# Performance work log

Hardware: AMD Instinct MI355X
Metric: run time of the kernel (lower is better)

The kernel has to match this reference:

```python
import jax, jax.numpy as jnp
import numpy as np

COMMITMENT_COST = 0.25


def setup_inputs() -> dict:
    key = jax.random.key(0)
    kx, ke = jax.random.split(key)
    x = jax.random.normal(kx, (16, 2048, 256), dtype=jnp.float32)
    embedding = jax.random.normal(ke, (4096, 256), dtype=jnp.float32)
    return {"x": x, "embedding": embedding}


def reference(x, embedding):
    # x: [B, T, D], embedding: [M, D]. Eval-mode VQ-EMA forward (no buffer updates).
    B, T, D = x.shape
    M = embedding.shape[0]
    x_flat = x.reshape(-1, D)  # [N, D], N = B*T

    distances = (
        jnp.sum(embedding * embedding, axis=1)[None, :]
        + jnp.sum(x_flat * x_flat, axis=1, keepdims=True)
        - 2.0 * (x_flat @ embedding.T)
    )
    indices = jnp.argmin(distances.astype(jnp.float32), axis=-1)  # [N]
    quantized = embedding[indices].reshape(x.shape)  # gather lookup, [B, T, D]

    # commitment loss, masked by nonpadding frames
    e_latent = (x - jax.lax.stop_gradient(quantized)) ** 2  # mse, reduction='none'
    nonpadding = (jnp.abs(x).sum(-1) > 0).astype(x.dtype)  # [B, T]
    e_latent_loss = (e_latent.mean(-1) * nonpadding).sum() / nonpadding.sum()
    loss = COMMITMENT_COST * e_latent_loss

    # straight-through estimator
    quantized_st = x + jax.lax.stop_gradient(quantized - x)

    # perplexity from code usage histogram (avoid materializing [N, M] one-hot)
    counts = jnp.zeros((M,), jnp.float32).at[indices].add(1.0)
    avg_probs = counts / indices.shape[0]
    perplexity = jnp.exp(-jnp.sum(avg_probs * jnp.log(avg_probs + 1e-10)))

    return quantized_st, loss, indices.reshape(B, T), perplexity
```

## Files before the change

### kernel.cpp

```cpp
#include <hip/hip_runtime.h>
#include <math.h>
#include <stdint.h>

#define D 256
#define N 32768
#define M 4096

#define LOSS_OFF 8388608
#define IDX_OFF  8388609
#define PERP_OFF 8421377

typedef _Float16 f16;
typedef _Float16 f16x8 __attribute__((ext_vector_type(8)));
typedef _Float16 f16x4 __attribute__((ext_vector_type(4)));
typedef float f32x4 __attribute__((ext_vector_type(4)));

#define WS_XH     0u
#define WS_XL     16777216u
#define WS_EH     33554432u
#define WS_EL     35651584u
#define WS_ENORM  37748736u
#define WS_COUNTS 37765120u
#define WS_IDX    37781504u
#define WS_CAND   37912576u
#define WS_LPART  38961152u
#define WS_NPART  38969344u
#define WS_NEEDED 38977536u
#define C_BLOCKS  2048

__device__ __forceinline__ void gload16(const void* g, void* l) {
    __builtin_amdgcn_global_load_lds(
        (const __attribute__((address_space(1))) uint32_t*)g,
        (__attribute__((address_space(3))) uint32_t*)l, 16, 0, 0);
}

#define MFMA16(a, b, c) __builtin_amdgcn_mfma_f32_16x16x32_f16((a), (b), (c), 0, 0, 0)

__global__ __launch_bounds__(256) void init_kernel(const float* __restrict__ emb,
                                                   float* __restrict__ enorm,
                                                   unsigned* __restrict__ counts) {
    int tid = threadIdx.x;
    int lane = tid & 63;
    int wid = tid >> 6;
    int m = blockIdx.x * 4 + wid;
    const float4* e4 = (const float4*)(emb + (size_t)m * D);
    float4 v = e4[lane];
    float s = v.x * v.x + v.y * v.y + v.z * v.z + v.w * v.w;
    #pragma unroll
    for (int off = 32; off; off >>= 1) s += __shfl_xor(s, off);
    if (lane == 0) enorm[m] = s;
    int gid = blockIdx.x * 256 + tid;
    if (gid < M) counts[gid] = 0u;
}

__global__ __launch_bounds__(256) void convert_kernel(const float* __restrict__ s,
                                                      f16* __restrict__ dh,
                                                      f16* __restrict__ dl, int n4) {
    int i = blockIdx.x * 256 + threadIdx.x;
    if (i >= n4) return;
    float4 v = ((const float4*)s)[i];
    f16 h0 = (f16)v.x, h1 = (f16)v.y, h2 = (f16)v.z, h3 = (f16)v.w;
    f16 l0 = (f16)(v.x - (float)h0), l1 = (f16)(v.y - (float)h1);
    f16 l2 = (f16)(v.z - (float)h2), l3 = (f16)(v.w - (float)h3);
    f16x4 hv; hv[0] = h0; hv[1] = h1; hv[2] = h2; hv[3] = h3;
    f16x4 lv; lv[0] = l0; lv[1] = l1; lv[2] = l2; lv[3] = l3;
    *(f16x4*)(dh + (size_t)i * 4) = hv;
    *(f16x4*)(dl + (size_t)i * 4) = lv;
}

__global__ __launch_bounds__(512) void argmin_xp(
    const f16* __restrict__ xh, const f16* __restrict__ xl,
    const f16* __restrict__ eh, const f16* __restrict__ el,
    const float* __restrict__ enorm, float2* __restrict__ cand)
{
    extern __shared__ char smem[];
    f16* Xh = (f16*)smem;
    f16* EBa = (f16*)(smem + 65536);
    float2 (*msm)[32] = (float2(*)[32])(smem + 65536);

    int tid = threadIdx.x;
    int lane = tid & 63;
    int wid = tid >> 6;
    int wr = wid >> 1;
    int wc = wid & 1;
    int b = blockIdx.x;
    int rb = (b & 7) * 32 + (b >> 5);
    int cs = (b >> 3) & 3;
    int row0 = rb * 128;
    int rxor = lane & 7;

    {
        int srow = lane >> 5, lslot = lane & 31;
        #pragma unroll
        for (int q = 0; q < 8; ++q) {
            int ch = wid * 8 + q;
            int row = ch * 2 + srow;
            int ss = lslot ^ (row & 7);
            gload16(xh + (size_t)(row0 + row) * D + ss * 8, smem + ch * 1024);
        }
    }
    {
        int srow = lane >> 3, lslot = lane & 7;
        int c0 = cs * 1024;
        #pragma unroll
        for (int q = 0; q < 2; ++q) {
            int ch = wid * 2 + q;
            int row = ch * 8 + srow;
            int ss = lslot ^ (row & 7);
            const f16* src = (ss < 4) ? eh : el;
            gload16(src + (size_t)(c0 + row) * D + (ss & 3) * 8,
                    smem + 65536 + ch * 1024);
        }
    }
    f16x8 xlr[2][8];
    #pragma unroll
    for (int i = 0; i < 2; ++i) {
        int row = row0 + wr * 32 + i * 16 + (lane & 15);
        #pragma unroll
        for (int kc = 0; kc < 8; ++kc)
            xlr[i][kc] = *(const f16x8*)(xl + (size_t)row * D + kc * 32 + (lane >> 4) * 8);
    }
    __syncthreads();

    float bestv[2][4];
    int bestc[2][4];
    #pragma unroll
    for (int i = 0; i < 2; ++i)
        #pragma unroll
        for (int r = 0; r < 4; ++r) { bestv[i][r] = 3.4e38f; bestc[i][r] = 0; }

    for (int ct = 0; ct < 8; ++ct) {
        int c0 = (cs * 8 + ct) * 128;
        f32x4 acc[2][4];
        #pragma unroll
        for (int i = 0; i < 2; ++i)
            #pragma unroll
            for (int j = 0; j < 4; ++j) acc[i][j] = (f32x4)0.0f;

        #pragma unroll
        for (int kc = 0; kc < 8; ++kc) {
            if (ct * 8 + kc < 63) {
                int t1 = ct * 8 + kc + 1;
                int ct1 = t1 >> 3, kc1 = t1 & 7, d1 = t1 & 1;
                int c01 = (cs * 8 + ct1) * 128;
                int srow = lane >> 3, lslot = lane & 7;
                #pragma unroll
                for (int q = 0; q < 2; ++q) {
                    int ch = wid * 2 + q;
                    int row = ch * 8 + srow;
                    int ss = lslot ^ (row & 7);
                    const f16* src = (ss < 4) ? eh : el;
                    gload16(src + (size_t)(c01 + row) * D + kc1 * 32 + (ss & 3) * 8,
                            smem + 65536 + d1 * 16384 + ch * 1024);
                }
            }
            {
                const f16* EB = EBa + (kc & 1) * 8192;
                f16x8 ah[2], bh[4], bl[4];
                #pragma unroll
                for (int i = 0; i < 2; ++i) {
                    int row = wr * 32 + i * 16 + (lane & 15);
                    int sl = (kc * 4 + (lane >> 4)) ^ rxor;
                    ah[i] = *(const f16x8*)(Xh + row * 256 + sl * 8);
                }
                #pragma unroll
                for (int j = 0; j < 4; ++j) {
                    int row = wc * 64 + j * 16 + (lane & 15);
                    const f16* ebr = EB + row * 64;
                    bh[j] = *(const f16x8*)(ebr + (((lane >> 4)) ^ rxor) * 8);
                    bl[j] = *(const f16x8*)(ebr + ((4 + (lane >> 4)) ^ rxor) * 8);
                }
                #pragma unroll
                for (int i = 0; i < 2; ++i)
                    #pragma unroll
                    for (int j = 0; j < 4; ++j)
                        acc[i][j] = MFMA16(ah[i], bh[j], acc[i][j]);
                #pragma unroll
                for (int i = 0; i < 2; ++i)
                    #pragma unroll
                    for (int j = 0; j < 4; ++j)
                        acc[i][j] = MFMA16(ah[i], bl[j], acc[i][j]);
                #pragma unroll
                for (int i = 0; i < 2; ++i)
                    #pragma unroll
                    for (int j = 0; j < 4; ++j)
                        acc[i][j] = MFMA16(xlr[i][kc], bh[j], acc[i][j]);
            }
            __syncthreads();
        }
        float enj[4];
        #pragma unroll
        for (int j = 0; j < 4; ++j) enj[j] = enorm[c0 + wc * 64 + j * 16 + (lane & 15)];
        #pragma unroll
        for (int i = 0; i < 2; ++i)
            #pragma unroll
            for (int j = 0; j < 4; ++j) {
                int c = c0 + wc * 64 + j * 16 + (lane & 15);
                #pragma unroll
                for (int r = 0; r < 4; ++r) {
                    float s = enj[j] - 2.0f * acc[i][j][r];
                    if (s < bestv[i][r]) { bestv[i][r] = s; bestc[i][r] = c; }
                }
            }
    }

    float rv[2][4]; int rc[2][4];
    #pragma unroll
    for (int i = 0; i < 2; ++i)
        #pragma unroll
        for (int r = 0; r < 4; ++r) {
            float v = bestv[i][r]; int c = bestc[i][r];
            #pragma unroll
            for (int off = 8; off; off >>= 1) {
                float ov = __shfl_xor(v, off);
                int oc = __shfl_xor(c, off);
                if (ov < v || (ov == v && oc < c)) { v = ov; c = oc; }
            }
            rv[i][r] = v; rc[i][r] = c;
            if ((lane & 15) == 0 && wc == 1) {
                int rloc = i * 16 + (lane >> 4) * 4 + r;
                float2 p; p.x = v; p.y = __int_as_float(c);
                msm[wr][rloc] = p;
            }
        }
    __syncthreads();
    if (wc == 0 && (lane & 15) == 0) {
        #pragma unroll
        for (int i = 0; i < 2; ++i)
            #pragma unroll
            for (int r = 0; r < 4; ++r) {
                int rloc = i * 16 + (lane >> 4) * 4 + r;
                float v = rv[i][r]; int c = rc[i][r];
                float2 o = msm[wr][rloc];
                float ov = o.x; int oc = __float_as_int(o.y);
                if (ov < v || (ov == v && oc < c)) { v = ov; c = oc; }
                float2 p; p.x = v; p.y = __int_as_float(c);
                cand[(size_t)cs * N + row0 + wr * 32 + rloc] = p;
            }
    }
}

__global__ __launch_bounds__(256) void merge_kernel(const float2* __restrict__ cand,
                                                    unsigned* __restrict__ counts,
                                                    int* __restrict__ idx_out,
                                                    float* __restrict__ idx_f) {
    int row = blockIdx.x * 256 + threadIdx.x;
    float bv = 3.4e38f; int bc = 0;
    #pragma unroll
    for (int cs = 0; cs < 4; ++cs) {
        float2 p = cand[(size_t)cs * N + row];
        int c = __float_as_int(p.y);
        if (p.x < bv || (p.x == bv && c < bc)) { bv = p.x; bc = c; }
    }
    idx_out[row] = bc;
    idx_f[row] = (float)bc;
    atomicAdd(&counts[bc], 1u);
}

#define BR 64
#define BC 128
#define BK 64
__global__ __launch_bounds__(256) void argmin_fp32(
    const float* __restrict__ x, const float* __restrict__ emb,
    const float* __restrict__ enorm, unsigned* __restrict__ counts,
    int* __restrict__ idx_out, float* __restrict__ idx_f)
{
    __shared__ float xs[BR][65];
    __shared__ float es[BC][65];
    __shared__ float en_s[BC];
    int tid = threadIdx.x;
    int ty = tid >> 4, tx = tid & 15;
    int r0 = blockIdx.x * BR;
    float bestv[4]; int bestc[4];
    #pragma unroll
    for (int i = 0; i < 4; ++i) { bestv[i] = 3.4e38f; bestc[i] = 0; }
    for (int ct = 0; ct < M / BC; ++ct) {
        int c0 = ct * BC;
        float acc[4][8];
        #pragma unroll
        for (int i = 0; i < 4; ++i)
            #pragma unroll
            for (int j = 0; j < 8; ++j) acc[i][j] = 0.0f;
        for (int kt = 0; kt < D / BK; ++kt) {
            __syncthreads();
            #pragma unroll
            for (int p = 0; p < 4; ++p) {
                int l = p * 256 + tid, r = l >> 4, k4 = l & 15;
                float4 v = *(const float4*)(x + (size_t)(r0 + r) * D + kt * BK + k4 * 4);
                xs[r][k4 * 4] = v.x; xs[r][k4 * 4 + 1] = v.y;
                xs[r][k4 * 4 + 2] = v.z; xs[r][k4 * 4 + 3] = v.w;
            }
            #pragma unroll
            for (int p = 0; p < 8; ++p) {
                int l = p * 256 + tid, r = l >> 4, k4 = l & 15;
                float4 v = *(const float4*)(emb + (size_t)(c0 + r) * D + kt * BK + k4 * 4);
                es[r][k4 * 4] = v.x; es[r][k4 * 4 + 1] = v.y;
                es[r][k4 * 4 + 2] = v.z; es[r][k4 * 4 + 3] = v.w;
            }
            if (kt == 0 && tid < BC) en_s[tid] = enorm[c0 + tid];
            __syncthreads();
            #pragma unroll 8
            for (int k = 0; k < BK; ++k) {
                float xv[4], ev[8];
                #pragma unroll
                for (int i = 0; i < 4; ++i) xv[i] = xs[ty + 16 * i][k];
                #pragma unroll
                for (int j = 0; j < 8; ++j) ev[j] = es[tx + 16 * j][k];
                #pragma unroll
                for (int i = 0; i < 4; ++i)
                    #pragma unroll
                    for (int j = 0; j < 8; ++j)
                        acc[i][j] = fmaf(xv[i], ev[j], acc[i][j]);
            }
        }
        #pragma unroll
        for (int i = 0; i < 4; ++i)
            #pragma unroll
            for (int j = 0; j < 8; ++j) {
                int c = c0 + tx + 16 * j;
                float s = en_s[tx + 16 * j] - 2.0f * acc[i][j];
                if (s < bestv[i]) { bestv[i] = s; bestc[i] = c; }
            }
    }
    #pragma unroll
    for (int i = 0; i < 4; ++i) {
        float v = bestv[i]; int c = bestc[i];
        #pragma unroll
        for (int off = 8; off; off >>= 1) {
            float ov = __shfl_xor(v, off, 16);
            int oc = __shfl_xor(c, off, 16);
            if (ov < v || (ov == v && oc < c)) { v = ov; c = oc; }
        }
        if (tx == 0) {
            int row = r0 + ty + 16 * i;
            idx_out[row] = c; idx_f[row] = (float)c;
            atomicAdd(&counts[c], 1u);
        }
    }
}

__global__ __launch_bounds__(256) void gather_kernel(
    const float* __restrict__ x, const float* __restrict__ emb,
    const int* __restrict__ idx, float* __restrict__ out,
    float* __restrict__ lpart, float* __restrict__ npart)
{
    int tid = threadIdx.x, lane = tid & 63, wid = tid >> 6;
    __shared__ float ls[4], ns[4];
    double lacc = 0.0, nacc = 0.0;
    for (int it = 0; it < 4; ++it) {
        int row = (blockIdx.x * 4 + wid) + it * (C_BLOCKS * 4);
        int c = idx[row];
        float4 xv = *(const float4*)(x + (size_t)row * D + lane * 4);
        float4 qv = *(const float4*)(emb + (size_t)c * D + lane * 4);
        float4 o;
        o.x = xv.x + (qv.x - xv.x); o.y = xv.y + (qv.y - xv.y);
        o.z = xv.z + (qv.z - xv.z); o.w = xv.w + (qv.w - xv.w);
        *(float4*)(out + (size_t)row * D + lane * 4) = o;
        float dx = xv.x - qv.x, dy = xv.y - qv.y, dz = xv.z - qv.z, dw = xv.w - qv.w;
        float ss = dx * dx + dy * dy + dz * dz + dw * dw;
        float sa = fabsf(xv.x) + fabsf(xv.y) + fabsf(xv.z) + fabsf(xv.w);
        #pragma unroll
        for (int off = 32; off; off >>= 1) {
            ss += __shfl_xor(ss, off);
            sa += __shfl_xor(sa, off);
        }
        if (sa > 0.0f) { lacc += (double)ss * (1.0 / 256.0); nacc += 1.0; }
    }
    if (lane == 0) { ls[wid] = (float)lacc; ns[wid] = (float)nacc; }
    __syncthreads();
    if (tid == 0) {
        lpart[blockIdx.x] = ls[0] + ls[1] + ls[2] + ls[3];
        npart[blockIdx.x] = ns[0] + ns[1] + ns[2] + ns[3];
    }
}

__global__ __launch_bounds__(256) void finalize_kernel(
    const unsigned* __restrict__ counts, const float* __restrict__ lpart,
    const float* __restrict__ npart, float* __restrict__ out)
{
    __shared__ double sd[256];
    __shared__ double sl[256];
    __shared__ double sn[256];
    int tid = threadIdx.x;
    double t = 0.0;
    for (int i = tid; i < M; i += 256) {
        double p = (double)counts[i] * (1.0 / 32768.0);
        t += p * log(p + 1e-10);
    }
    sd[tid] = t;
    double ln = 0.0, nn = 0.0;
    for (int i = tid; i < C_BLOCKS; i += 256) { ln += lpart[i]; nn += npart[i]; }
    sl[tid] = ln; sn[tid] = nn;
    __syncthreads();
    for (int s = 128; s; s >>= 1) {
        if (tid < s) { sd[tid] += sd[tid + s]; sl[tid] += sl[tid + s]; sn[tid] += sn[tid + s]; }
        __syncthreads();
    }
    if (tid == 0) {
        out[PERP_OFF] = (float)exp(-sd[0]);
        out[LOSS_OFF] = (float)(0.25 * sl[0] / sn[0]);
    }
}

extern "C" void kernel_launch(void* const* d_in, const int* in_sizes, int n_in,
                              void* d_out, int out_size, void* d_ws, size_t ws_size,
                              hipStream_t stream) {
    const float* x = (const float*)d_in[0];
    const float* emb = (const float*)d_in[1];
    float* out = (float*)d_out;
    char* ws = (char*)d_ws;

    float* enorm = (float*)(ws + WS_ENORM);
    unsigned* counts = (unsigned*)(ws + WS_COUNTS);
    int* idx = (int*)(ws + WS_IDX);
    float* lpart = (float*)(ws + WS_LPART);
    float* npart = (float*)(ws + WS_NPART);

    if (ws_size >= (size_t)WS_NEEDED) {
        f16* xh = (f16*)(ws + WS_XH);
        f16* xl = (f16*)(ws + WS_XL);
        f16* eh = (f16*)(ws + WS_EH);
        f16* el = (f16*)(ws + WS_EL);
        float2* cand = (float2*)(ws + WS_CAND);

        init_kernel<<<M / 4, 256, 0, stream>>>(emb, enorm, counts);
        convert_kernel<<<(N * D / 4) / 256, 256, 0, stream>>>(x, xh, xl, N * D / 4);
        convert_kernel<<<(M * D / 4) / 256, 256, 0, stream>>>(emb, eh, el, M * D / 4);
        argmin_xp<<<1024, 512, 98304, stream>>>(xh, xl, eh, el, enorm, cand);
        merge_kernel<<<N / 256, 256, 0, stream>>>(cand, counts, idx, out + IDX_OFF);
    } else {
        enorm = (float*)(ws + 0);
        counts = (unsigned*)(ws + 16384);
        idx = (int*)(ws + 32768);
        lpart = (float*)(ws + 163840);
        npart = (float*)(ws + 172032);
        init_kernel<<<M / 4, 256, 0, stream>>>(emb, enorm, counts);
        argmin_fp32<<<N / BR, 256, 0, stream>>>(x, emb, enorm, counts, idx, out + IDX_OFF);
    }
    gather_kernel<<<C_BLOCKS, 256, 0, stream>>>(x, emb, idx, out, lpart, npart);
    finalize_kernel<<<1, 256, 0, stream>>>(counts, lpart, npart, out);
}
```

Before: 322.6 us.

## Convert x to hi/lo fp16 in registers and fuse merge into gather

The argmin kernel now reads fp32 x directly and splits it into fp16 hi/lo register fragments, which removes the separate x conversion pass and its workspace traffic. The codebook tiles are staged in 128-wide K halves with double buffering across a 128KB LDS allocation, cutting the number of barriers per column tile from eight to two. The candidate merge is folded into the gather/loss kernel, which drops one launch and the intermediate index buffer. In exchange the larger LDS footprint and the extra x registers may limit occupancy despite the launch bound of 2.

```diff
diff --git a/kernel.cpp b/kernel.cpp
--- a/kernel.cpp
+++ b/kernel.cpp
@@ -68,15 +68,13 @@
     *(f16x4*)(dl + (size_t)i * 4) = lv;
 }
 
-__global__ __launch_bounds__(512) void argmin_xp(
-    const f16* __restrict__ xh, const f16* __restrict__ xl,
-    const f16* __restrict__ eh, const f16* __restrict__ el,
-    const float* __restrict__ enorm, float2* __restrict__ cand)
+__global__ __launch_bounds__(512, 2) void argmin_xr(
+    const float* __restrict__ x, const f16* __restrict__ eh,
+    const f16* __restrict__ el, const float* __restrict__ enorm,
+    float2* __restrict__ cand)
 {
     extern __shared__ char smem[];
-    f16* Xh = (f16*)smem;
-    f16* EBa = (f16*)(smem + 65536);
-    float2 (*msm)[32] = (float2(*)[32])(smem + 65536);
+    float2 (*msm)[32] = (float2(*)[32])smem;
 
     int tid = threadIdx.x;
     int lane = tid & 63;
@@ -90,35 +88,34 @@
     int rxor = lane & 7;
 
     {
-        int srow = lane >> 5, lslot = lane & 31;
         #pragma unroll
         for (int q = 0; q < 8; ++q) {
-            int ch = wid * 8 + q;
-            int row = ch * 2 + srow;
-            int ss = lslot ^ (row & 7);
-            gload16(xh + (size_t)(row0 + row) * D + ss * 8, smem + ch * 1024);
-        }
-    }
-    {
-        int srow = lane >> 3, lslot = lane & 7;
-        int c0 = cs * 1024;
-        #pragma unroll
-        for (int q = 0; q < 2; ++q) {
-            int ch = wid * 2 + q;
-            int row = ch * 8 + srow;
-            int ss = lslot ^ (row & 7);
-            const f16* src = (ss < 4) ? eh : el;
-            gload16(src + (size_t)(c0 + row) * D + (ss & 3) * 8,
-                    smem + 65536 + ch * 1024);
-        }
-    }
-    f16x8 xlr[2][8];
+            int cb = q * 8 + wid;
+            int row = (cb * 4 + (lane >> 4)) & 127;
+            int ks = ((lane & 15) ^ (row & 7)) * 8;
+            const f16* src = (cb >> 5) ? el : eh;
+            gload16(src + (size_t)(cs * 1024 + row) * D + ks, smem + cb * 1024);
+        }
+    }
+    f16x8 xhr[2][8], xlr[2][8];
     #pragma unroll
     for (int i = 0; i < 2; ++i) {
-        int row = row0 + wr * 32 + i * 16 + (lane & 15);
-        #pragma unroll
-        for (int kc = 0; kc < 8; ++kc)
-            xlr[i][kc] = *(const f16x8*)(xl + (size_t)row * D + kc * 32 + (lane >> 4) * 8);
+        const float* xr = x + (size_t)(row0 + wr * 32 + i * 16 + (lane & 15)) * D;
+        #pragma unroll
+        for (int kc = 0; kc < 8; ++kc) {
+            float4 v0 = *(const float4*)(xr + kc * 32 + (lane >> 4) * 8);
+            float4 v1 = *(const float4*)(xr + kc * 32 + (lane >> 4) * 8 + 4);
+            f16x8 h, l;
+            h[0] = (f16)v0.x; l[0] = (f16)(v0.x - (float)h[0]);
+            h[1] = (f16)v0.y; l[1] = (f16)(v0.y - (float)h[1]);
+            h[2] = (f16)v0.z; l[2] = (f16)(v0.z - (float)h[2]);
+            h[3] = (f16)v0.w; l[3] = (f16)(v0.w - (float)h[3]);
+            h[4] = (f16)v1.x; l[4] = (f16)(v1.x - (float)h[4]);
+            h[5] = (f16)v1.y; l[5] = (f16)(v1.y - (float)h[5]);
+            h[6] = (f16)v1.z; l[6] = (f16)(v1.z - (float)h[6]);
+            h[7] = (f16)v1.w; l[7] = (f16)(v1.w - (float)h[7]);
+            xhr[i][kc] = h; xlr[i][kc] = l;
+        }
     }
     __syncthreads();
 
@@ -138,53 +135,47 @@
             for (int j = 0; j < 4; ++j) acc[i][j] = (f32x4)0.0f;
 
         #pragma unroll
-        for (int kc = 0; kc < 8; ++kc) {
-            if (ct * 8 + kc < 63) {
-                int t1 = ct * 8 + kc + 1;
-                int ct1 = t1 >> 3, kc1 = t1 & 7, d1 = t1 & 1;
+        for (int kh = 0; kh < 2; ++kh) {
+            if (kh == 0 || ct < 7) {
+                int ct1 = (kh == 0) ? ct : ct + 1;
+                int kh1 = kh ^ 1;
                 int c01 = (cs * 8 + ct1) * 128;
-                int srow = lane >> 3, lslot = lane & 7;
-                #pragma unroll
-                for (int q = 0; q < 2; ++q) {
-                    int ch = wid * 2 + q;
-                    int row = ch * 8 + srow;
-                    int ss = lslot ^ (row & 7);
-                    const f16* src = (ss < 4) ? eh : el;
-                    gload16(src + (size_t)(c01 + row) * D + kc1 * 32 + (ss & 3) * 8,
-                            smem + 65536 + d1 * 16384 + ch * 1024);
+                char* dst = smem + (kh ^ 1) * 65536;
+                #pragma unroll
+                for (int q = 0; q < 8; ++q) {
+                    int cb = q * 8 + wid;
+                    int row = (cb * 4 + (lane >> 4)) & 127;
+                    int ks = (((lane & 15) ^ (row & 7)) * 8) + kh1 * 128;
+                    const f16* src = (cb >> 5) ? el : eh;
+                    gload16(src + (size_t)(c01 + row) * D + ks, dst + cb * 1024);
                 }
             }
-            {
-                const f16* EB = EBa + (kc & 1) * 8192;
-                f16x8 ah[2], bh[4], bl[4];
-                #pragma unroll
-                for (int i = 0; i < 2; ++i) {
-                    int row = wr * 32 + i * 16 + (lane & 15);
-                    int sl = (kc * 4 + (lane >> 4)) ^ rxor;
-                    ah[i] = *(const f16x8*)(Xh + row * 256 + sl * 8);
-                }
+            const f16* EB = (const f16*)(smem + kh * 65536);
+            #pragma unroll
+            for (int kq = 0; kq < 4; ++kq) {
+                f16x8 bh[4], bl[4];
                 #pragma unroll
                 for (int j = 0; j < 4; ++j) {
-                    int row = wc * 64 + j * 16 + (lane & 15);
-                    const f16* ebr = EB + row * 64;
-                    bh[j] = *(const f16x8*)(ebr + (((lane >> 4)) ^ rxor) * 8);
-                    bl[j] = *(const f16x8*)(ebr + ((4 + (lane >> 4)) ^ rxor) * 8);
+                    int brow = wc * 64 + j * 16 + (lane & 15);
+                    int sw = (kq * 4 + (lane >> 4)) ^ rxor;
+                    bh[j] = *(const f16x8*)(EB + brow * 128 + sw * 8);
+                    bl[j] = *(const f16x8*)(EB + 16384 + brow * 128 + sw * 8);
                 }
                 #pragma unroll
                 for (int i = 0; i < 2; ++i)
                     #pragma unroll
                     for (int j = 0; j < 4; ++j)
-                        acc[i][j] = MFMA16(ah[i], bh[j], acc[i][j]);
+                        acc[i][j] = MFMA16(xhr[i][kh * 4 + kq], bh[j], acc[i][j]);
                 #pragma unroll
                 for (int i = 0; i < 2; ++i)
                     #pragma unroll
                     for (int j = 0; j < 4; ++j)
-                        acc[i][j] = MFMA16(ah[i], bl[j], acc[i][j]);
+                        acc[i][j] = MFMA16(xhr[i][kh * 4 + kq], bl[j], acc[i][j]);
                 #pragma unroll
                 for (int i = 0; i < 2; ++i)
                     #pragma unroll
                     for (int j = 0; j < 4; ++j)
-                        acc[i][j] = MFMA16(xlr[i][kc], bh[j], acc[i][j]);
+                        acc[i][j] = MFMA16(xlr[i][kh * 4 + kq], bh[j], acc[i][j]);
             }
             __syncthreads();
         }
@@ -240,21 +231,51 @@
     }
 }
 
-__global__ __launch_bounds__(256) void merge_kernel(const float2* __restrict__ cand,
-                                                    unsigned* __restrict__ counts,
-                                                    int* __restrict__ idx_out,
-                                                    float* __restrict__ idx_f) {
-    int row = blockIdx.x * 256 + threadIdx.x;
-    float bv = 3.4e38f; int bc = 0;
-    #pragma unroll
-    for (int cs = 0; cs < 4; ++cs) {
-        float2 p = cand[(size_t)cs * N + row];
-        int c = __float_as_int(p.y);
-        if (p.x < bv || (p.x == bv && c < bc)) { bv = p.x; bc = c; }
-    }
-    idx_out[row] = bc;
-    idx_f[row] = (float)bc;
-    atomicAdd(&counts[bc], 1u);
+__global__ __launch_bounds__(256) void gather_merge(
+    const float* __restrict__ x, const float* __restrict__ emb,
+    const float2* __restrict__ cand, float* __restrict__ out,
+    float* __restrict__ idx_f, unsigned* __restrict__ counts,
+    float* __restrict__ lpart, float* __restrict__ npart)
+{
+    int tid = threadIdx.x, lane = tid & 63, wid = tid >> 6;
+    __shared__ float ls[4], ns[4];
+    double lacc = 0.0, nacc = 0.0;
+    for (int it = 0; it < 4; ++it) {
+        int row = (blockIdx.x * 4 + wid) + it * (C_BLOCKS * 4);
+        float bv = 3.4e38f; int bc = 0;
+        #pragma unroll
+        for (int cs = 0; cs < 4; ++cs) {
+            float2 p = cand[(size_t)cs * N + row];
+            int cc = __float_as_int(p.y);
+            if (p.x < bv || (p.x == bv && cc < bc)) { bv = p.x; bc = cc; }
+        }
+        if (lane == 0) {
+            idx_f[row] = (float)bc;
+            atomicAdd(&counts[bc], 1u);
+        }
+        int c = bc;
+        float4 xv = *(const float4*)(x + (size_t)row * D + lane * 4);
+        float4 qv = *(const float4*)(emb + (size_t)c * D + lane * 4);
+        float4 o;
+        o.x = xv.x + (qv.x - xv.x); o.y = xv.y + (qv.y - xv.y);
+        o.z = xv.z + (qv.z - xv.z); o.w = xv.w + (qv.w - xv.w);
+        *(float4*)(out + (size_t)row * D + lane * 4) = o;
+        float dx = xv.x - qv.x, dy = xv.y - qv.y, dz = xv.z - qv.z, dw = xv.w - qv.w;
+        float ss = dx * dx + dy * dy + dz * dz + dw * dw;
+        float sa = fabsf(xv.x) + fabsf(xv.y) + fabsf(xv.z) + fabsf(xv.w);
+        #pragma unroll
+        for (int off = 32; off; off >>= 1) {
+            ss += __shfl_xor(ss, off);
+            sa += __shfl_xor(sa, off);
+        }
+        if (sa > 0.0f) { lacc += (double)ss * (1.0 / 256.0); nacc += 1.0; }
+    }
+    if (lane == 0) { ls[wid] = (float)lacc; ns[wid] = (float)nacc; }
+    __syncthreads();
+    if (tid == 0) {
+        lpart[blockIdx.x] = ls[0] + ls[1] + ls[2] + ls[3];
+        npart[blockIdx.x] = ns[0] + ns[1] + ns[2] + ns[3];
+    }
 }
 
 #define BR 64
@@ -412,31 +433,28 @@
 
     float* enorm = (float*)(ws + WS_ENORM);
     unsigned* counts = (unsigned*)(ws + WS_COUNTS);
-    int* idx = (int*)(ws + WS_IDX);
     float* lpart = (float*)(ws + WS_LPART);
     float* npart = (float*)(ws + WS_NPART);
 
     if (ws_size >= (size_t)WS_NEEDED) {
-        f16* xh = (f16*)(ws + WS_XH);
-        f16* xl = (f16*)(ws + WS_XL);
         f16* eh = (f16*)(ws + WS_EH);
         f16* el = (f16*)(ws + WS_EL);
         float2* cand = (float2*)(ws + WS_CAND);
 
         init_kernel<<<M / 4, 256, 0, stream>>>(emb, enorm, counts);
-        convert_kernel<<<(N * D / 4) / 256, 256, 0, stream>>>(x, xh, xl, N * D / 4);
         convert_kernel<<<(M * D / 4) / 256, 256, 0, stream>>>(emb, eh, el, M * D / 4);
-        argmin_xp<<<1024, 512, 98304, stream>>>(xh, xl, eh, el, enorm, cand);
-        merge_kernel<<<N / 256, 256, 0, stream>>>(cand, counts, idx, out + IDX_OFF);
+        argmin_xr<<<1024, 512, 131072, stream>>>(x, eh, el, enorm, cand);
+        gather_merge<<<C_BLOCKS, 256, 0, stream>>>(x, emb, cand, out, out + IDX_OFF,
+                                                   counts, lpart, npart);
     } else {
         enorm = (float*)(ws + 0);
         counts = (unsigned*)(ws + 16384);
-        idx = (int*)(ws + 32768);
+        int* idx = (int*)(ws + 32768);
         lpart = (float*)(ws + 163840);
         npart = (float*)(ws + 172032);
         init_kernel<<<M / 4, 256, 0, stream>>>(emb, enorm, counts);
         argmin_fp32<<<N / BR, 256, 0, stream>>>(x, emb, enorm, counts, idx, out + IDX_OFF);
-    }
-    gather_kernel<<<C_BLOCKS, 256, 0, stream>>>(x, emb, idx, out, lpart, npart);
+        gather_kernel<<<C_BLOCKS, 256, 0, stream>>>(x, emb, idx, out, lpart, npart);
+    }
     finalize_kernel<<<1, 256, 0, stream>>>(counts, lpart, npart, out);
 }
```

Result: slower. 339.7 us (+5.3%).
